# Performance work log

Hardware: AMD Instinct MI355X
Metric: run time of the kernel (lower is better)

## Reference

```python
import jax, jax.numpy as jnp
import numpy as np


def dct2_mat(N):
    # Orthonormal DCT-II matrix M[k, n]; scipy dct(norm='ortho') == M @ x,
    # and since M is orthogonal, idct(norm='ortho') == M.T @ x.
    n = jnp.arange(N, dtype=jnp.float32)
    k = jnp.arange(N, dtype=jnp.float32)[:, None]
    M = jnp.cos(jnp.pi * (n + 0.5) * k / N)
    scale = jnp.where(k == 0, jnp.sqrt(1.0 / N), jnp.sqrt(2.0 / N))
    return (M * scale).astype(jnp.float32)


def setup_inputs() -> dict:
    key = jax.random.key(0)
    x = jax.random.normal(key, (8, 32, 64, 64, 64), dtype=jnp.float32)
    return {"x": x}


def reference(x):
    # Faithful to original: DCT is applied along B, D, H (axes 0,1,2 of the
    # permuted [B,D,H,W,C] tensor), crop/pad acts on D,H,W, then IDCT along B,D,H.
    OUT = (32, 32, 32)
    TR = (32, 32, 32)
    B, C, D, H, W = x.shape
    CB, CD, CH = dct2_mat(B), dct2_mat(D), dct2_mat(H)

    # forward DCT-II (ortho) along B, D, H as batched matmuls
    y = jnp.einsum('kb,bcdhw->kcdhw', CB, x)
    y = jnp.einsum('kd,bcdhw->bckhw', CD, y)
    y = jnp.einsum('kh,bcdhw->bcdkw', CH, y)

    # spectral crop along D, H, W, then zero-pad up to output_size
    y = y[:, :, :TR[0], :TR[1], :TR[2]]
    y = jnp.pad(y, ((0, 0), (0, 0),
                    (0, OUT[0] - TR[0]),
                    (0, OUT[1] - TR[1]),
                    (0, OUT[2] - TR[2])))

    # inverse DCT (ortho) = transpose of the (orthogonal) DCT matrix
    Bi, Di, Hi = y.shape[0], y.shape[2], y.shape[3]
    z = jnp.einsum('kn,kcdhw->ncdhw', dct2_mat(Bi), y)
    z = jnp.einsum('kn,bckhw->bcnhw', dct2_mat(Di), z)
    z = jnp.einsum('kn,bcdkw->bcdnw', dct2_mat(Hi), z)
    return z
```

## Files before the change

kernel.cpp:

```cpp
#include <hip/hip_runtime.h>
#include <math.h>


__global__ void build_A_kernel(float* __restrict__ A, float* __restrict__ At) {
  int idx = blockIdx.x * blockDim.x + threadIdx.x;
  if (idx >= 32 * 64) return;
  int n = idx >> 6;
  int h = idx & 63;
  const float s32a = sqrtf(1.0f / 32.0f), s32b = sqrtf(2.0f / 32.0f);
  const float s64a = sqrtf(1.0f / 64.0f), s64b = sqrtf(2.0f / 64.0f);
  float s = 0.0f;
  for (int k = 0; k < 32; ++k) {
    float c32 = cosf((float)M_PI * ((float)n + 0.5f) * (float)k / 32.0f) * ((k == 0) ? s32a : s32b);
    float c64 = cosf((float)M_PI * ((float)h + 0.5f) * (float)k / 64.0f) * ((k == 0) ? s64a : s64b);
    s = fmaf(c32, c64, s);
  }
  A[n * 64 + h] = s;
  At[h * 32 + n] = s;
}

__global__ __launch_bounds__(512, 4) void spectral_kernel(
    const float* __restrict__ x, const float* __restrict__ A,
    const float* __restrict__ At, float* __restrict__ out) {
  __shared__ float V[16][32][32];

  const int tid = threadIdx.x;
  const int bc = blockIdx.x;
  const int wv = tid >> 6;
  const int dloc = (tid >> 5) & 1;
  const int w = tid & 31;
  const int nhq = (tid >> 4) & 3;
  const int w16 = tid & 15;

  const float* xb = x + (size_t)bc * 262144;

  float acc[4][8][2];
  #pragma unroll
  for (int i = 0; i < 4; ++i)
    #pragma unroll
    for (int j = 0; j < 8; ++j) {
      acc[i][j][0] = 0.f;
      acc[i][j][1] = 0.f;
    }

  #pragma unroll 1
  for (int cc = 0; cc < 4; ++cc) {
    const int d = cc * 16 + wv * 2 + dloc;
    const float* xcol = xb + (size_t)d * 4096 + w;

    float p[32];
    #pragma unroll
    for (int nh = 0; nh < 32; ++nh) p[nh] = 0.f;

    #pragma unroll 1
    for (int hc = 0; hc < 8; ++hc) {
      float xr[8];
      #pragma unroll
      for (int i = 0; i < 8; ++i) xr[i] = xcol[(hc * 8 + i) * 64];
      #pragma unroll
      for (int nh = 0; nh < 32; ++nh) {
        const float* Arow = A + nh * 64 + hc * 8;
        float q0 = fmaf(Arow[0], xr[0], fmaf(Arow[1], xr[1], 0.f));
        float q1 = fmaf(Arow[2], xr[2], fmaf(Arow[3], xr[3], 0.f));
        float q2 = fmaf(Arow[4], xr[4], fmaf(Arow[5], xr[5], 0.f));
        float q3 = fmaf(Arow[6], xr[6], fmaf(Arow[7], xr[7], 0.f));
        p[nh] += (q0 + q1) + (q2 + q3);
      }
    }
    #pragma unroll
    for (int nh = 0; nh < 32; ++nh) V[wv * 2 + dloc][nh][w] = p[nh];
    __syncthreads();

    #pragma unroll 1
    for (int dd = 0; dd < 16; ++dd) {
      const int dg = cc * 16 + dd;
      const float* Acol = At + dg * 32 + wv * 4;
      const float a0 = Acol[0], a1 = Acol[1], a2 = Acol[2], a3 = Acol[3];
      #pragma unroll
      for (int j = 0; j < 8; ++j) {
        const float v0 = V[dd][j * 4 + nhq][w16 * 2 + 0];
        const float v1 = V[dd][j * 4 + nhq][w16 * 2 + 1];
        acc[0][j][0] = fmaf(a0, v0, acc[0][j][0]);
        acc[0][j][1] = fmaf(a0, v1, acc[0][j][1]);
        acc[1][j][0] = fmaf(a1, v0, acc[1][j][0]);
        acc[1][j][1] = fmaf(a1, v1, acc[1][j][1]);
        acc[2][j][0] = fmaf(a2, v0, acc[2][j][0]);
        acc[2][j][1] = fmaf(a2, v1, acc[2][j][1]);
        acc[3][j][0] = fmaf(a3, v0, acc[3][j][0]);
        acc[3][j][1] = fmaf(a3, v1, acc[3][j][1]);
      }
    }
    __syncthreads();
  }

  float* ob = out + (size_t)bc * 32768;
  #pragma unroll
  for (int i = 0; i < 4; ++i) {
    const int nd = wv * 4 + i;
    #pragma unroll
    for (int j = 0; j < 8; ++j) {
      const int nh = j * 4 + nhq;
      float2 v;
      v.x = acc[i][j][0];
      v.y = acc[i][j][1];
      *(float2*)(ob + nd * 1024 + nh * 32 + w16 * 2) = v;
    }
  }
}

extern "C" void kernel_launch(void* const* d_in, const int* in_sizes, int n_in,
                              void* d_out, int out_size, void* d_ws, size_t ws_size,
                              hipStream_t stream) {
  const float* x = (const float*)d_in[0];
  float* A = (float*)d_ws;
  float* At = A + 2048;
  build_A_kernel<<<2, 1024, 0, stream>>>(A, At);
  spectral_kernel<<<256, 512, 0, stream>>>(x, A, At, (float*)d_out);
}
```

Measured before the change: 382.7 us.

## Double block size to 1024 threads and software-prefetch x rows in stage one

```diff
diff --git a/kernel.cpp b/kernel.cpp
--- a/kernel.cpp
+++ b/kernel.cpp
@@ -19,75 +19,84 @@
   At[h * 32 + n] = s;
 }
 
-__global__ __launch_bounds__(512, 4) void spectral_kernel(
+__global__ __launch_bounds__(1024, 4) void spectral_kernel(
     const float* __restrict__ x, const float* __restrict__ A,
     const float* __restrict__ At, float* __restrict__ out) {
-  __shared__ float V[16][32][32];
+  __shared__ float V[32][32][32];
 
   const int tid = threadIdx.x;
   const int bc = blockIdx.x;
   const int wv = tid >> 6;
-  const int dloc = (tid >> 5) & 1;
+  const int dloc = tid >> 5;
   const int w = tid & 31;
   const int nhq = (tid >> 4) & 3;
   const int w16 = tid & 15;
+  const int ndg = wv & 7;
+  const int jg = wv >> 3;
 
   const float* xb = x + (size_t)bc * 262144;
 
-  float acc[4][8][2];
+  float acc[4][4][2];
   #pragma unroll
   for (int i = 0; i < 4; ++i)
     #pragma unroll
-    for (int j = 0; j < 8; ++j) {
+    for (int j = 0; j < 4; ++j) {
       acc[i][j][0] = 0.f;
       acc[i][j][1] = 0.f;
     }
 
   #pragma unroll 1
-  for (int cc = 0; cc < 4; ++cc) {
-    const int d = cc * 16 + wv * 2 + dloc;
+  for (int cc = 0; cc < 2; ++cc) {
+    const int d = cc * 32 + dloc;
     const float* xcol = xb + (size_t)d * 4096 + w;
 
     float p[32];
     #pragma unroll
     for (int nh = 0; nh < 32; ++nh) p[nh] = 0.f;
 
+    float cur[16], nxt[16];
+    #pragma unroll
+    for (int i = 0; i < 16; ++i) cur[i] = xcol[i * 64];
+
     #pragma unroll 1
-    for (int hc = 0; hc < 8; ++hc) {
-      float xr[8];
-      #pragma unroll
-      for (int i = 0; i < 8; ++i) xr[i] = xcol[(hc * 8 + i) * 64];
+    for (int hc = 0; hc < 4; ++hc) {
+      if (hc < 3) {
+        #pragma unroll
+        for (int i = 0; i < 16; ++i) nxt[i] = xcol[(hc * 16 + 16 + i) * 64];
+      }
       #pragma unroll
       for (int nh = 0; nh < 32; ++nh) {
-        const float* Arow = A + nh * 64 + hc * 8;
-        float q0 = fmaf(Arow[0], xr[0], fmaf(Arow[1], xr[1], 0.f));
-        float q1 = fmaf(Arow[2], xr[2], fmaf(Arow[3], xr[3], 0.f));
-        float q2 = fmaf(Arow[4], xr[4], fmaf(Arow[5], xr[5], 0.f));
-        float q3 = fmaf(Arow[6], xr[6], fmaf(Arow[7], xr[7], 0.f));
-        p[nh] += (q0 + q1) + (q2 + q3);
+        const float* Ar = A + nh * 64 + hc * 16;
+        float s = p[nh];
+        #pragma unroll
+        for (int i = 0; i < 16; ++i) s = fmaf(Ar[i], cur[i], s);
+        p[nh] = s;
       }
+      #pragma unroll
+      for (int i = 0; i < 16; ++i) cur[i] = nxt[i];
     }
+
     #pragma unroll
-    for (int nh = 0; nh < 32; ++nh) V[wv * 2 + dloc][nh][w] = p[nh];
+    for (int nh = 0; nh < 32; ++nh) V[dloc][nh][w] = p[nh];
     __syncthreads();
 
     #pragma unroll 1
-    for (int dd = 0; dd < 16; ++dd) {
-      const int dg = cc * 16 + dd;
-      const float* Acol = At + dg * 32 + wv * 4;
+    for (int dd = 0; dd < 32; ++dd) {
+      const int dg = cc * 32 + dd;
+      const float* Acol = At + dg * 32 + ndg * 4;
       const float a0 = Acol[0], a1 = Acol[1], a2 = Acol[2], a3 = Acol[3];
       #pragma unroll
-      for (int j = 0; j < 8; ++j) {
-        const float v0 = V[dd][j * 4 + nhq][w16 * 2 + 0];
-        const float v1 = V[dd][j * 4 + nhq][w16 * 2 + 1];
-        acc[0][j][0] = fmaf(a0, v0, acc[0][j][0]);
-        acc[0][j][1] = fmaf(a0, v1, acc[0][j][1]);
-        acc[1][j][0] = fmaf(a1, v0, acc[1][j][0]);
-        acc[1][j][1] = fmaf(a1, v1, acc[1][j][1]);
-        acc[2][j][0] = fmaf(a2, v0, acc[2][j][0]);
-        acc[2][j][1] = fmaf(a2, v1, acc[2][j][1]);
-        acc[3][j][0] = fmaf(a3, v0, acc[3][j][0]);
-        acc[3][j][1] = fmaf(a3, v1, acc[3][j][1]);
+      for (int j = 0; j < 4; ++j) {
+        const int nh = (jg * 4 + j) * 4 + nhq;
+        const float2 v = *(const float2*)&V[dd][nh][w16 * 2];
+        acc[0][j][0] = fmaf(a0, v.x, acc[0][j][0]);
+        acc[0][j][1] = fmaf(a0, v.y, acc[0][j][1]);
+        acc[1][j][0] = fmaf(a1, v.x, acc[1][j][0]);
+        acc[1][j][1] = fmaf(a1, v.y, acc[1][j][1]);
+        acc[2][j][0] = fmaf(a2, v.x, acc[2][j][0]);
+        acc[2][j][1] = fmaf(a2, v.y, acc[2][j][1]);
+        acc[3][j][0] = fmaf(a3, v.x, acc[3][j][0]);
+        acc[3][j][1] = fmaf(a3, v.y, acc[3][j][1]);
       }
     }
     __syncthreads();
@@ -96,10 +105,10 @@
   float* ob = out + (size_t)bc * 32768;
   #pragma unroll
   for (int i = 0; i < 4; ++i) {
-    const int nd = wv * 4 + i;
+    const int nd = ndg * 4 + i;
     #pragma unroll
-    for (int j = 0; j < 8; ++j) {
-      const int nh = j * 4 + nhq;
+    for (int j = 0; j < 4; ++j) {
+      const int nh = (jg * 4 + j) * 4 + nhq;
       float2 v;
       v.x = acc[i][j][0];
       v.y = acc[i][j][1];
@@ -114,6 +123,6 @@
   const float* x = (const float*)d_in[0];
   float* A = (float*)d_ws;
   float* At = A + 2048;
-  build_A_kernel<<<2, 1024, 0, stream>>>(A, At);
-  spectral_kernel<<<256, 512, 0, stream>>>(x, A, At, (float*)d_out);
+  build_A_kernel<<<32, 64, 0, stream>>>(A, At);
+  spectral_kernel<<<256, 1024, 0, stream>>>(x, A, At, (float*)d_out);
 }
```

Measured after the change: 368.3 us. 3.8% less time.
